# Optimization experiments

Hardware: AMD Instinct MI355X
Metric: run time of the kernel (lower is better)

## Reference

```python
import jax, jax.numpy as jnp
from jax import lax
import numpy as np

H_SIZE = 1024      # max(hidden_size_list)
EXPAND = 2
INTER = EXPAND * H_SIZE            # 2048 intermediate size
NHEADS = 32                        # max(num_heads_list)
HEAD_DIM = INTER // NHEADS         # 64
NSTATE = 128                       # ssm state size
NGROUPS = 1
KCONV = 4                          # conv kernel
CHUNK = 256                        # chunk size for SSD scan
EPS = 1e-5                         # layer_norm_epsilon
CONV_DIM = INTER + 2 * NGROUPS * NSTATE        # 2304
PROJ_DIM = 2 * INTER + 2 * NGROUPS * NSTATE + NHEADS  # 4352


def setup_inputs() -> dict:
    key = jax.random.key(0)
    ks = jax.random.split(key, 9)
    B, S = 2, 4096
    return {
        "hidden_states": jax.random.normal(ks[0], (B, S, H_SIZE), jnp.float32),
        "in_proj_w": jax.random.normal(ks[1], (PROJ_DIM, H_SIZE), jnp.float32) * 0.02,
        "conv_w": jax.random.normal(ks[2], (CONV_DIM, 1, KCONV), jnp.float32) * 0.2,
        "conv_b": jax.random.normal(ks[3], (CONV_DIM,), jnp.float32) * 0.02,
        "dt_bias": jax.random.normal(ks[4], (NHEADS,), jnp.float32) * 0.1,
        "A_log": jax.random.uniform(ks[5], (NHEADS,), jnp.float32, 0.0, 1.0),
        "D": jax.random.normal(ks[6], (NHEADS,), jnp.float32),
        "norm_w": jnp.ones((INTER,), jnp.float32) + 0.01 * jax.random.normal(ks[7], (INTER,), jnp.float32),
        "out_proj_w": jax.random.normal(ks[8], (H_SIZE, INTER), jnp.float32) * 0.02,
    }


def _segsum(a):
    # a: [B,H,C,L] -> lower-triangular segment sums [B,H,C,L,L]
    L = a.shape[-1]
    cs = jnp.cumsum(a, axis=-1)
    ss = cs[..., :, None] - cs[..., None, :]
    mask = jnp.tril(jnp.ones((L, L), dtype=bool))
    return jnp.where(mask, ss, -jnp.inf)


def reference(hidden_states, in_proj_w, conv_w, conv_b, dt_bias, A_log, D, norm_w, out_proj_w):
    B, S, _ = hidden_states.shape
    proj = hidden_states @ in_proj_w.T                       # [B,S,4352]
    gate = proj[..., :INTER]                                 # [B,S,2048]
    hBC = proj[..., INTER:INTER + CONV_DIM]                  # [B,S,2304]
    dt = proj[..., INTER + CONV_DIM:]                        # [B,S,H]

    # causal depthwise conv1d + SiLU
    xc_ = jnp.transpose(hBC, (0, 2, 1))                      # [B,C,S]
    xc_ = lax.conv_general_dilated(xc_, conv_w, (1,), [(KCONV - 1, 0)],
                                   dimension_numbers=('NCH', 'OIH', 'NCH'),
                                   feature_group_count=CONV_DIM)
    xc_ = jax.nn.silu(xc_ + conv_b[None, :, None])
    hBC = jnp.transpose(xc_, (0, 2, 1))                      # [B,S,2304]

    h = hBC[..., :INTER]
    Bm = hBC[..., INTER:INTER + NGROUPS * NSTATE]
    Cm = hBC[..., INTER + NGROUPS * NSTATE:]

    dt = jax.nn.softplus(dt + dt_bias)                       # [B,S,H]
    dt = jnp.clip(dt, 0.0, None)                             # time_step_limit (0, inf)
    A = -jnp.exp(A_log)                                      # [H]

    NC = S // CHUNK
    xh = h.reshape(B, NC, CHUNK, NHEADS, HEAD_DIM)
    Bh = jnp.repeat(Bm.reshape(B, NC, CHUNK, NGROUPS, NSTATE), NHEADS // NGROUPS, axis=3)
    Ch = jnp.repeat(Cm.reshape(B, NC, CHUNK, NGROUPS, NSTATE), NHEADS // NGROUPS, axis=3)
    dtc = dt.reshape(B, NC, CHUNK, NHEADS)

    a = jnp.transpose(dtc * A, (0, 3, 1, 2))                 # [B,H,NC,L]
    A_cum = jnp.cumsum(a, axis=-1)                           # [B,H,NC,L]
    Lmat = jnp.exp(_segsum(a))                               # [B,H,NC,L,L]
    xdt = xh * dtc[..., None]                                # [B,NC,L,H,P]

    # intra-chunk (diagonal block) output
    Yd = jnp.einsum('bclhn,bcshn,bhcls,bcshp->bclhp', Ch, Bh, Lmat, xdt)

    # per-chunk final states
    decay = jnp.exp(A_cum[..., -1:] - A_cum)                 # [B,H,NC,L]
    states = jnp.einsum('bclhn,bhcl,bclhp->bchpn', Bh, decay, xdt)  # [B,NC,H,P,N]

    # inter-chunk recurrence over chunks
    g = jnp.exp(A_cum[..., -1])                              # [B,H,NC]
    def step(carry, inp):
        s_c, g_c = inp
        return carry * g_c[..., None, None] + s_c, carry
    _, prev = lax.scan(step, jnp.zeros((B, NHEADS, HEAD_DIM, NSTATE), states.dtype),
                       (jnp.moveaxis(states, 1, 0), jnp.moveaxis(g, 2, 0)))
    prev = jnp.moveaxis(prev, 0, 1)                          # [B,NC,H,P,N] state entering each chunk

    Yo = jnp.einsum('bclhn,bchpn,bhcl->bclhp', Ch, prev, jnp.exp(A_cum))

    y = (Yd + Yo + D[None, None, None, :, None] * xh).reshape(B, S, INTER)

    # gated RMSNorm (fp32 internally)
    yf = y.astype(jnp.float32) * jax.nn.silu(gate.astype(jnp.float32))
    var = jnp.mean(yf * yf, axis=-1, keepdims=True)
    y = norm_w * (yf * lax.rsqrt(var + EPS))

    return y @ out_proj_w.T
```

## Files before the change

### kernel.cpp

```cpp
#include <hip/hip_runtime.h>
#include <hip/hip_bf16.h>
#include <math.h>

#define H_SIZE   1024
#define INTER    2048
#define NHEADS   32
#define HEAD_DIM 64
#define NSTATE   128
#define KCONV    4
#define CHUNK    256
#define CONV_DIM (INTER + 2*NSTATE)
#define CIN_DIM  (CONV_DIM + NHEADS)
#define PROJ_DIM (2*INTER + 2*NSTATE + NHEADS)
#define BATCH    2
#define SEQ      4096
#define NC       (SEQ/CHUNK)
#define EPS_F    1e-5f

typedef __attribute__((ext_vector_type(8))) short bf16x8;
typedef __attribute__((ext_vector_type(4))) float f32x4;
typedef unsigned short ushort_t;

__device__ __forceinline__ ushort_t f2bf(float x) {
  unsigned u = __float_as_uint(x);
  u += 0x7fffu + ((u >> 16) & 1u);
  return (ushort_t)(u >> 16);
}
__device__ __forceinline__ float bf2f(ushort_t h) {
  return __uint_as_float((unsigned)h << 16);
}

__global__ __launch_bounds__(256) void convert_hl_kernel(
    const float* __restrict__ x, ushort_t* __restrict__ hi,
    ushort_t* __restrict__ lo, int n4) {
  int idx = blockIdx.x * 256 + threadIdx.x;
  int stride = gridDim.x * 256;
  for (int i = idx; i < n4; i += stride) {
    const float* p = x + (size_t)i * 4;
    float v0 = p[0], v1 = p[1], v2 = p[2], v3 = p[3];
    ushort_t h0 = f2bf(v0), h1 = f2bf(v1), h2 = f2bf(v2), h3 = f2bf(v3);
    ushort_t l0 = f2bf(v0 - bf2f(h0));
    ushort_t l1 = f2bf(v1 - bf2f(h1));
    ushort_t l2 = f2bf(v2 - bf2f(h2));
    ushort_t l3 = f2bf(v3 - bf2f(h3));
    *(uint2*)(hi + (size_t)i * 4) =
        make_uint2((unsigned)h0 | ((unsigned)h1 << 16), (unsigned)h2 | ((unsigned)h3 << 16));
    *(uint2*)(lo + (size_t)i * 4) =
        make_uint2((unsigned)l0 | ((unsigned)l1 << 16), (unsigned)l2 | ((unsigned)l3 << 16));
  }
}

__global__ __launch_bounds__(256) void convert_bc_kernel(
    const float* __restrict__ hbc, ushort_t* __restrict__ Bph,
    ushort_t* __restrict__ Bpl, ushort_t* __restrict__ Cph,
    ushort_t* __restrict__ Cpl) {
  const int n4 = (BATCH*SEQ) * 64;
  int idx = blockIdx.x * 256 + threadIdx.x;
  int stride = gridDim.x * 256;
  for (int i = idx; i < n4; i += stride) {
    int row = i >> 6;
    int c4 = (i & 63) * 4;
    float4 v = *(const float4*)(hbc + (size_t)row*CONV_DIM + INTER + c4);
    ushort_t h0 = f2bf(v.x), h1 = f2bf(v.y), h2 = f2bf(v.z), h3 = f2bf(v.w);
    ushort_t l0 = f2bf(v.x - bf2f(h0)), l1 = f2bf(v.y - bf2f(h1));
    ushort_t l2 = f2bf(v.z - bf2f(h2)), l3 = f2bf(v.w - bf2f(h3));
    uint2 hp = make_uint2((unsigned)h0 | ((unsigned)h1 << 16), (unsigned)h2 | ((unsigned)h3 << 16));
    uint2 lp = make_uint2((unsigned)l0 | ((unsigned)l1 << 16), (unsigned)l2 | ((unsigned)l3 << 16));
    if (c4 < 128) {
      *(uint2*)(Bph + (size_t)row*128 + c4) = hp;
      *(uint2*)(Bpl + (size_t)row*128 + c4) = lp;
    } else {
      *(uint2*)(Cph + (size_t)row*128 + (c4 - 128)) = hp;
      *(uint2*)(Cpl + (size_t)row*128 + (c4 - 128)) = lp;
    }
  }
}

#define LROW 40
__global__ __launch_bounds__(256) void gemm_hl_mfma_kernel(
    const ushort_t* __restrict__ Ahi, const ushort_t* __restrict__ Alo,
    const ushort_t* __restrict__ Whi, const ushort_t* __restrict__ Wlo,
    float* __restrict__ C, int M, int N, int K, int nx) {
  __shared__ __align__(16) ushort_t Ah[128*LROW], Al[128*LROW];
  __shared__ __align__(16) ushort_t Wh[128*LROW], Wl[128*LROW];
  const int tid = threadIdx.x;
  const int lane = tid & 63, wid = tid >> 6;
  const int wr = wid >> 1, wc = wid & 1;
  const int fr = lane & 15, fg = lane >> 4;

  const int cpx = gridDim.x >> 3;
  const int logical = (blockIdx.x & 7) * cpx + (blockIdx.x >> 3);
  const int grp = logical / (nx * 4);
  const int rem = logical - grp * (nx * 4);
  const int bx = rem >> 2;
  const int by = grp * 4 + (rem & 3);
  const int m0 = by * 128, n0 = bx * 128;

  const int r0 = tid >> 2;
  const int kseg = (tid & 3) * 8;
  const int r1 = r0 + 64;
  const size_t a0 = (size_t)(m0 + r0) * K + kseg;
  const size_t a1 = (size_t)(m0 + r1) * K + kseg;
  const size_t w0 = (size_t)(n0 + r0) * K + kseg;
  const size_t w1 = (size_t)(n0 + r1) * K + kseg;
  const bool wv0 = (n0 + r0) < N, wv1 = (n0 + r1) < N;

  bf16x8 gA0, gA1, gAl0, gAl1, gW0, gW1, gWl0, gWl1;
  const bf16x8 z8 = {};
  f32x4 acc[4][4] = {};

  auto glod = [&](int k0) {
    gA0  = *(const bf16x8*)(Ahi + a0 + k0);
    gA1  = *(const bf16x8*)(Ahi + a1 + k0);
    gAl0 = *(const bf16x8*)(Alo + a0 + k0);
    gAl1 = *(const bf16x8*)(Alo + a1 + k0);
    gW0  = wv0 ? *(const bf16x8*)(Whi + w0 + k0) : z8;
    gW1  = wv1 ? *(const bf16x8*)(Whi + w1 + k0) : z8;
    gWl0 = wv0 ? *(const bf16x8*)(Wlo + w0 + k0) : z8;
    gWl1 = wv1 ? *(const bf16x8*)(Wlo + w1 + k0) : z8;
  };

  glod(0);
  for (int k0 = 0; k0 < K; k0 += 32) {
    __syncthreads();
    *(bf16x8*)&Ah[r0*LROW + kseg] = gA0;
    *(bf16x8*)&Ah[r1*LROW + kseg] = gA1;
    *(bf16x8*)&Al[r0*LROW + kseg] = gAl0;
    *(bf16x8*)&Al[r1*LROW + kseg] = gAl1;
    *(bf16x8*)&Wh[r0*LROW + kseg] = gW0;
    *(bf16x8*)&Wh[r1*LROW + kseg] = gW1;
    *(bf16x8*)&Wl[r0*LROW + kseg] = gWl0;
    *(bf16x8*)&Wl[r1*LROW + kseg] = gWl1;
    __syncthreads();
    if (k0 + 32 < K) glod(k0 + 32);

    bf16x8 wh[4], wl[4];
#pragma unroll
    for (int nf = 0; nf < 4; ++nf) {
      int off = (wc*64 + nf*16 + fr) * LROW + 8*fg;
      wh[nf] = *(const bf16x8*)&Wh[off];
      wl[nf] = *(const bf16x8*)&Wl[off];
    }
#pragma unroll
    for (int mf = 0; mf < 4; ++mf) {
      int aoff = (wr*64 + mf*16 + fr) * LROW + 8*fg;
      bf16x8 ah = *(const bf16x8*)&Ah[aoff];
      bf16x8 al = *(const bf16x8*)&Al[aoff];
#pragma unroll
      for (int nf = 0; nf < 4; ++nf) {
        acc[mf][nf] = __builtin_amdgcn_mfma_f32_16x16x32_bf16(ah, wh[nf], acc[mf][nf], 0, 0, 0);
        acc[mf][nf] = __builtin_amdgcn_mfma_f32_16x16x32_bf16(ah, wl[nf], acc[mf][nf], 0, 0, 0);
        acc[mf][nf] = __builtin_amdgcn_mfma_f32_16x16x32_bf16(al, wh[nf], acc[mf][nf], 0, 0, 0);
      }
    }
  }

#pragma unroll
  for (int mf = 0; mf < 4; ++mf)
#pragma unroll
    for (int nf = 0; nf < 4; ++nf) {
      int col = n0 + wc*64 + nf*16 + fr;
      if (col < N) {
        size_t base = (size_t)(m0 + wr*64 + mf*16 + fg*4) * N + col;
        f32x4 v = acc[mf][nf];
        C[base]               = v[0];
        C[base + (size_t)N]   = v[1];
        C[base + 2*(size_t)N] = v[2];
        C[base + 3*(size_t)N] = v[3];
      }
    }
}

__global__ __launch_bounds__(256) void conv_kernel(
    const float* __restrict__ cin, const float* __restrict__ cw,
    const float* __restrict__ cb, const float* __restrict__ dtb,
    float* __restrict__ hbc, float* __restrict__ dtp) {
  const int bs = blockIdx.x;
  const int b = bs / SEQ, s = bs % SEQ;
  const int tid = threadIdx.x;
  const float* base = cin + (size_t)b * SEQ * CIN_DIM;
  for (int c = tid; c < CONV_DIM; c += 256) {
    float acc = cb[c];
#pragma unroll
    for (int k = 0; k < KCONV; ++k) {
      int sp = s - (KCONV-1) + k;
      if (sp >= 0) acc = fmaf(cw[c*KCONV + k], base[(size_t)sp * CIN_DIM + c], acc);
    }
    acc = acc / (1.f + expf(-acc));
    hbc[(size_t)bs * CONV_DIM + c] = acc;
  }
  if (tid < NHEADS) {
    float d = cin[(size_t)bs * CIN_DIM + CONV_DIM + tid] + dtb[tid];
    d = (d > 20.f) ? d : log1pf(expf(d));
    dtp[(size_t)bs * NHEADS + tid] = d;
  }
}

__global__ __launch_bounds__(256) void cumsum_kernel(
    const float* __restrict__ dtp, const float* __restrict__ A_log,
    float* __restrict__ acum, float* __restrict__ gch) {
  const int c = blockIdx.x, h = blockIdx.y, b = blockIdx.z;
  const int tid = threadIdx.x;
  __shared__ float sm[CHUNK];
  const float A = -expf(A_log[h]);
  const int s = c * CHUNK + tid;
  float a = dtp[(size_t)(b*SEQ + s)*NHEADS + h] * A;
  sm[tid] = a;
  __syncthreads();
  for (int off = 1; off < CHUNK; off <<= 1) {
    float v = 0.f;
    if (tid >= off) v = sm[tid - off];
    __syncthreads();
    sm[tid] += v;
    __syncthreads();
  }
  float ac = sm[tid];
  acum[((size_t)(b*NHEADS + h)*NC + c)*CHUNK + tid] = ac;
  if (tid == CHUNK-1) gch[(size_t)(b*NHEADS + h)*NC + c] = expf(ac);
}

#define CBROW 136
#define XROW2 72
__global__ __launch_bounds__(256) void yd_mfma_kernel(
    const ushort_t* __restrict__ Bph, const ushort_t* __restrict__ Bpl,
    const ushort_t* __restrict__ Cph, const ushort_t* __restrict__ Cpl,
    const float* __restrict__ hbc, const float* __restrict__ acum,
    const float* __restrict__ dtp, const float* __restrict__ Dv,
    float* __restrict__ y) {
  __shared__ __align__(16) ushort_t BhS[64*CBROW], BlS[64*CBROW];
  __shared__ __align__(16) ushort_t XhS[64*XROW2], XlS[64*XROW2];
  __shared__ __align__(16) ushort_t GhS[4][16*XROW2], GlS[4][16*XROW2];
  __shared__ float acLs[64], acSs[64];

  const int h = blockIdx.x;
  const int c = blockIdx.y >> 2, lt = blockIdx.y & 3;
  const int b = blockIdx.z;
  const int tid = threadIdx.x;
  const int lane = tid & 63, w = tid >> 6;
  const int fr = lane & 15, fg = lane >> 4;

  const size_t seqbase = (size_t)(b*SEQ + c*CHUNK);
  const size_t acbase  = ((size_t)(b*NHEADS + h)*NC + c)*CHUNK;

  bf16x8 cfh[4], cfl[4];
  {
    const size_t cg = (seqbase + lt*64 + w*16 + fr) * 128;
#pragma unroll
    for (int ks = 0; ks < 4; ++ks) {
      int ko = ks*32 + fg*8;
      cfh[ks] = *(const bf16x8*)(Cph + cg + ko);
      cfl[ks] = *(const bf16x8*)(Cpl + cg + ko);
    }
  }
  if (tid < 64) acLs[tid] = acum[acbase + lt*64 + tid];

  f32x4 acc[4] = {};

  for (int st = 0; st <= lt; ++st) {
    __syncthreads();
    {
      const size_t g0 = (seqbase + st*64) * 128;
#pragma unroll
      for (int i = 0; i < 4; ++i) {
        int f = tid + 256*i; int r = f >> 4; int k8 = (f & 15) * 8;
        *(bf16x8*)&BhS[r*CBROW + k8] = *(const bf16x8*)(Bph + g0 + (size_t)r*128 + k8);
        *(bf16x8*)&BlS[r*CBROW + k8] = *(const bf16x8*)(Bpl + g0 + (size_t)r*128 + k8);
      }
    }
#pragma unroll
    for (int i = 0; i < 4; ++i) {
      int f = tid + 256*i; int s = f >> 4; int p0 = (f & 15) * 4;
      size_t row = seqbase + st*64 + s;
      float dtv = dtp[row*NHEADS + h];
      float4 xv = *(const float4*)(hbc + row*CONV_DIM + h*HEAD_DIM + p0);
      float vals[4] = {xv.x*dtv, xv.y*dtv, xv.z*dtv, xv.w*dtv};
#pragma unroll
      for (int j = 0; j < 4; ++j) {
        int p = p0 + j;
        int sw = s ^ (((p >> 2) & 7) << 3);
        ushort_t hh = f2bf(vals[j]);
        ushort_t ll = f2bf(vals[j] - bf2f(hh));
        XhS[p*XROW2 + sw] = hh;
        XlS[p*XROW2 + sw] = ll;
      }
    }
    if (tid < 64) acSs[tid] = acum[acbase + st*64 + tid];
    __syncthreads();

    f32x4 g[4] = {};
#pragma unroll
    for (int ks = 0; ks < 4; ++ks) {
      const int ko = ks*32 + fg*8;
#pragma unroll
      for (int nf = 0; nf < 4; ++nf) {
        const int rb = (nf*16 + fr) * CBROW + ko;
        bf16x8 bh = *(const bf16x8*)&BhS[rb];
        bf16x8 bl = *(const bf16x8*)&BlS[rb];
        g[nf] = __builtin_amdgcn_mfma_f32_16x16x32_bf16(cfh[ks], bh, g[nf], 0, 0, 0);
        g[nf] = __builtin_amdgcn_mfma_f32_16x16x32_bf16(cfh[ks], bl, g[nf], 0, 0, 0);
        g[nf] = __builtin_amdgcn_mfma_f32_16x16x32_bf16(cfl[ks], bh, g[nf], 0, 0, 0);
      }
    }
    {
      const bool full = (st < lt);
#pragma unroll
      for (int nf = 0; nf < 4; ++nf) {
        int sl = nf*16 + fr;
        float aS = acSs[sl];
#pragma unroll
        for (int r = 0; r < 4; ++r) {
          int ll = w*16 + fg*4 + r;
          float v = 0.f;
          if (full || ll >= sl) v = g[nf][r] * __expf(acLs[ll] - aS);
          ushort_t hh = f2bf(v);
          ushort_t lo2 = f2bf(v - bf2f(hh));
          GhS[w][(fg*4 + r)*XROW2 + sl] = hh;
          GlS[w][(fg*4 + r)*XROW2 + sl] = lo2;
        }
      }
    }
    __syncthreads();
#pragma unroll
    for (int ks = 0; ks < 2; ++ks) {
      const int ko = ks*32 + fg*8;
      bf16x8 gh = *(const bf16x8*)&GhS[w][fr*XROW2 + ko];
      bf16x8 gl = *(const bf16x8*)&GlS[w][fr*XROW2 + ko];
#pragma unroll
      for (int nf = 0; nf < 4; ++nf) {
        int p = nf*16 + fr;
        int kb = ko ^ (((p >> 2) & 7) << 3);
        bf16x8 xh = *(const bf16x8*)&XhS[p*XROW2 + kb];
        bf16x8 xl = *(const bf16x8*)&XlS[p*XROW2 + kb];
        acc[nf] = __builtin_amdgcn_mfma_f32_16x16x32_bf16(gh, xh, acc[nf], 0, 0, 0);
        acc[nf] = __builtin_amdgcn_mfma_f32_16x16x32_bf16(gh, xl, acc[nf], 0, 0, 0);
        acc[nf] = __builtin_amdgcn_mfma_f32_16x16x32_bf16(gl, xh, acc[nf], 0, 0, 0);
      }
    }
  }

  const float Dh = Dv[h];
#pragma unroll
  for (int nf = 0; nf < 4; ++nf) {
    int p = nf*16 + fr;
#pragma unroll
    for (int r = 0; r < 4; ++r) {
      size_t row = seqbase + lt*64 + w*16 + fg*4 + r;
      float xval = hbc[row*CONV_DIM + h*HEAD_DIM + p];
      y[row*INTER + h*HEAD_DIM + p] = acc[nf][r] + Dh * xval;
    }
  }
}

#define SXROW 72
__global__ __launch_bounds__(256) void states_mfma_kernel(
    const ushort_t* __restrict__ Bph, const ushort_t* __restrict__ Bpl,
    const float* __restrict__ hbc, const float* __restrict__ acum,
    const float* __restrict__ dtp, float* __restrict__ states) {
  __shared__ __align__(16) ushort_t XhS[64*SXROW], XlS[64*SXROW];
  __shared__ __align__(16) ushort_t BhS[128*SXROW], BlS[128*SXROW];
  const int h = blockIdx.x, c = blockIdx.y, b = blockIdx.z;
  const int tid = threadIdx.x;
  const int lane = tid & 63, w = tid >> 6;
  const int fr = lane & 15, fg = lane >> 4;
  const size_t seqbase = (size_t)(b*SEQ + c*CHUNK);
  const size_t acbase  = ((size_t)(b*NHEADS + h)*NC + c)*CHUNK;
  const float aclast = acum[acbase + CHUNK - 1];
  f32x4 acc[8] = {};

  for (int lt = 0; lt < 4; ++lt) {
    __syncthreads();
#pragma unroll
    for (int i = 0; i < 4; ++i) {
      int f = tid + 256*i; int l = f >> 4; int p0 = (f & 15) * 4;
      size_t row = seqbase + lt*64 + l;
      float mult = dtp[row*NHEADS + h] * __expf(aclast - acum[acbase + lt*64 + l]);
      float4 xv = *(const float4*)(hbc + row*CONV_DIM + h*HEAD_DIM + p0);
      float vals[4] = {xv.x*mult, xv.y*mult, xv.z*mult, xv.w*mult};
#pragma unroll
      for (int j = 0; j < 4; ++j) {
        int p = p0 + j;
        int sw = l ^ (((p >> 2) & 7) << 3);
        ushort_t hh = f2bf(vals[j]);
        XhS[p*SXROW + sw] = hh;
        XlS[p*SXROW + sw] = f2bf(vals[j] - bf2f(hh));
      }
    }
#pragma unroll
    for (int i = 0; i < 4; ++i) {
      int f = tid + 256*i; int l = f >> 4; int n8 = (f & 15) * 8;
      size_t g0 = (seqbase + lt*64 + l) * 128 + n8;
      bf16x8 bh = *(const bf16x8*)(Bph + g0);
      bf16x8 bl = *(const bf16x8*)(Bpl + g0);
#pragma unroll
      for (int j = 0; j < 8; ++j) {
        int n = n8 + j;
        int sw = l ^ (((n >> 2) & 7) << 3);
        BhS[n*SXROW + sw] = (ushort_t)bh[j];
        BlS[n*SXROW + sw] = (ushort_t)bl[j];
      }
    }
    __syncthreads();
#pragma unroll
    for (int ks = 0; ks < 2; ++ks) {
      const int ko = ks*32 + fg*8;
      const int pa = w*16 + fr;
      const int ka = ko ^ (((pa >> 2) & 7) << 3);
      bf16x8 ah = *(const bf16x8*)&XhS[pa*SXROW + ka];
      bf16x8 al = *(const bf16x8*)&XlS[pa*SXROW + ka];
#pragma unroll
      for (int nf = 0; nf < 8; ++nf) {
        const int nb = nf*16 + fr;
        const int kb = ko ^ (((nb >> 2) & 7) << 3);
        bf16x8 bh = *(const bf16x8*)&BhS[nb*SXROW + kb];
        bf16x8 bl = *(const bf16x8*)&BlS[nb*SXROW + kb];
        acc[nf] = __builtin_amdgcn_mfma_f32_16x16x32_bf16(ah, bh, acc[nf], 0, 0, 0);
        acc[nf] = __builtin_amdgcn_mfma_f32_16x16x32_bf16(ah, bl, acc[nf], 0, 0, 0);
        acc[nf] = __builtin_amdgcn_mfma_f32_16x16x32_bf16(al, bh, acc[nf], 0, 0, 0);
      }
    }
  }
  float* sp = states + ((size_t)(b*NC + c)*NHEADS + h)*HEAD_DIM*NSTATE;
#pragma unroll
  for (int nf = 0; nf < 8; ++nf) {
    int n = nf*16 + fr;
#pragma unroll
    for (int r = 0; r < 4; ++r) {
      int p = w*16 + fg*4 + r;
      sp[(size_t)p*NSTATE + n] = acc[nf][r];
    }
  }
}

__global__ __launch_bounds__(256) void scan_kernel(
    float* __restrict__ st, const float* __restrict__ g) {
  const int bh = blockIdx.x;
  const int b = bh >> 5, h = bh & 31;
  const int tid = threadIdx.x;
  float carry[32];
#pragma unroll
  for (int i = 0; i < 32; ++i) carry[i] = 0.f;
  for (int c = 0; c < NC; ++c) {
    const float gc = g[(size_t)(b*NHEADS + h)*NC + c];
    float* base = st + ((size_t)(b*NC + c)*NHEADS + h)*HEAD_DIM*NSTATE;
    ushort_t* ub = (ushort_t*)base;
    float sv[32];
#pragma unroll
    for (int i = 0; i < 32; ++i) sv[i] = base[i*256 + tid];
    __syncthreads();
#pragma unroll
    for (int i = 0; i < 32; ++i) {
      int e = i*256 + tid;
      ushort_t hh = f2bf(carry[i]);
      ub[e]        = hh;
      ub[8192 + e] = f2bf(carry[i] - bf2f(hh));
      carry[i] = fmaf(carry[i], gc, sv[i]);
    }
  }
}

#define PROW 136
__global__ __launch_bounds__(256) void yo_mfma_kernel(
    const ushort_t* __restrict__ Cph, const ushort_t* __restrict__ Cpl,
    const ushort_t* __restrict__ stp, const float* __restrict__ acum,
    float* __restrict__ y) {
  __shared__ __align__(16) ushort_t PhS[64*PROW], PlS[64*PROW];
  const int h = blockIdx.x, c = blockIdx.y, b = blockIdx.z;
  const int tid = threadIdx.x;
  const int lane = tid & 63, w = tid >> 6;
  const int fr = lane & 15, fg = lane >> 4;
  const size_t seqbase = (size_t)(b*SEQ + c*CHUNK);
  const size_t acbase  = ((size_t)(b*NHEADS + h)*NC + c)*CHUNK;

  const ushort_t* pb = stp + ((size_t)(b*NC + c)*NHEADS + h) * (size_t)(2*HEAD_DIM*NSTATE);
#pragma unroll
  for (int i = 0; i < 4; ++i) {
    int f = tid + 256*i; int r = f >> 4; int k8 = (f & 15) * 8;
    *(bf16x8*)&PhS[r*PROW + k8] = *(const bf16x8*)(pb + (size_t)r*128 + k8);
    *(bf16x8*)&PlS[r*PROW + k8] = *(const bf16x8*)(pb + 8192 + (size_t)r*128 + k8);
  }
  __syncthreads();

  for (int lt = 0; lt < 4; ++lt) {
    const size_t cg = (seqbase + lt*64 + w*16 + fr) * 128;
    f32x4 acc[4] = {};
#pragma unroll
    for (int ks = 0; ks < 4; ++ks) {
      int ko = ks*32 + fg*8;
      bf16x8 ah = *(const bf16x8*)(Cph + cg + ko);
      bf16x8 al = *(const bf16x8*)(Cpl + cg + ko);
#pragma unroll
      for (int nf = 0; nf < 4; ++nf) {
        const int rb = (nf*16 + fr) * PROW + ko;
        bf16x8 bh = *(const bf16x8*)&PhS[rb];
        bf16x8 bl = *(const bf16x8*)&PlS[rb];
        acc[nf] = __builtin_amdgcn_mfma_f32_16x16x32_bf16(ah, bh, acc[nf], 0, 0, 0);
        acc[nf] = __builtin_amdgcn_mfma_f32_16x16x32_bf16(ah, bl, acc[nf], 0, 0, 0);
        acc[nf] = __builtin_amdgcn_mfma_f32_16x16x32_bf16(al, bh, acc[nf], 0, 0, 0);
      }
    }
#pragma unroll
    for (int r = 0; r < 4; ++r) {
      int lrow = lt*64 + w*16 + fg*4 + r;
      float e = __expf(acum[acbase + lrow]);
      float* yrow = y + (seqbase + lrow)*INTER + h*HEAD_DIM;
#pragma unroll
      for (int nf = 0; nf < 4; ++nf) {
        int p = nf*16 + fr;
        yrow[p] += e * acc[nf][r];
      }
    }
  }
}

__global__ __launch_bounds__(256) void rms_kernel(
    float* __restrict__ y, const float* __restrict__ gate,
    const float* __restrict__ norm_w) {
  const int bs = blockIdx.x;
  const int tid = threadIdx.x;
  float* yrow = y + (size_t)bs * INTER;
  const float* grow = gate + (size_t)bs * INTER;
  float yf[8];
  float ss = 0.f;
#pragma unroll
  for (int i = 0; i < 8; ++i) {
    int c = tid + i*256;
    float v = yrow[c];
    float gt = grow[c];
    float f = v * (gt / (1.f + expf(-gt)));
    yf[i] = f;
    ss += f*f;
  }
#pragma unroll
  for (int off = 32; off >= 1; off >>= 1) ss += __shfl_xor(ss, off, 64);
  __shared__ float red[4];
  if ((tid & 63) == 0) red[tid >> 6] = ss;
  __syncthreads();
  float total = red[0] + red[1] + red[2] + red[3];
  float sc = rsqrtf(total * (1.f/INTER) + EPS_F);
#pragma unroll
  for (int i = 0; i < 8; ++i) {
    int c = tid + i*256;
    yrow[c] = norm_w[c] * yf[i] * sc;
  }
}

__global__ void zero_kernel(float* p, size_t n) {
  size_t i = (size_t)blockIdx.x * blockDim.x + threadIdx.x;
  if (i < n) p[i] = 0.f;
}

extern "C" void kernel_launch(void* const* d_in, const int* in_sizes, int n_in,
                              void* d_out, int out_size, void* d_ws, size_t ws_size,
                              hipStream_t stream) {
  const float* hidden = (const float*)d_in[0];
  const float* in_w   = (const float*)d_in[1];
  const float* conv_w = (const float*)d_in[2];
  const float* conv_b = (const float*)d_in[3];
  const float* dt_b   = (const float*)d_in[4];
  const float* A_log  = (const float*)d_in[5];
  const float* Dv     = (const float*)d_in[6];
  const float* norm_w = (const float*)d_in[7];
  const float* out_w  = (const float*)d_in[8];
  float* out = (float*)d_out;

  const int M = BATCH*SEQ;

  const size_t sz_cin  = (size_t)M * CIN_DIM;
  const size_t sz_hbc  = (size_t)M * CONV_DIM;
  const size_t sz_dtp  = (size_t)M * NHEADS;
  const size_t sz_acum = (size_t)BATCH*NHEADS*NC*CHUNK;
  const size_t sz_gch  = (size_t)BATCH*NHEADS*NC;
  const size_t sz_R    = (size_t)BATCH*NC*NHEADS*HEAD_DIM*NSTATE;
  const size_t need = (sz_cin + sz_hbc + sz_dtp + sz_acum + sz_gch + sz_R) * sizeof(float);

  if (ws_size < need) {
    size_t n = (size_t)out_size;
    zero_kernel<<<(unsigned)((n + 255) / 256), 256, 0, stream>>>(out, n);
    return;
  }

  float* ws = (float*)d_ws;
  size_t o = 0;
  float* cin  = ws + o; o += sz_cin;
  float* hbc  = ws + o; o += sz_hbc;
  float* dtp  = ws + o; o += sz_dtp;
  float* acum = ws + o; o += sz_acum;
  float* gch  = ws + o; o += sz_gch;
  float* R    = ws + o; o += sz_R;

  float* y    = cin;
  float* gate = hbc;
  float* st   = R;

  ushort_t* hidhi = (ushort_t*)R;
  ushort_t* hidlo = hidhi + (size_t)M * H_SIZE;
  ushort_t* yhi   = (ushort_t*)hbc;
  ushort_t* ylo   = yhi + (size_t)M * INTER;

  ushort_t* wscr = (ushort_t*)out;
  const size_t MP = (size_t)M * 128;
  ushort_t* bcp  = (ushort_t*)((char*)d_out + (size_t)(16u << 20));
  ushort_t* Bph = bcp;
  ushort_t* Bpl = bcp + MP;
  ushort_t* Cph = bcp + 2*MP;
  ushort_t* Cpl = bcp + 3*MP;

  {
    int nA4 = (M * H_SIZE) / 4;
    int nW  = CIN_DIM * H_SIZE;
    int nx = (CIN_DIM + 127) / 128;
    convert_hl_kernel<<<2048, 256, 0, stream>>>(hidden, hidhi, hidlo, nA4);
    convert_hl_kernel<<<2048, 256, 0, stream>>>(in_w + (size_t)INTER*H_SIZE, wscr, wscr + nW, nW/4);
    gemm_hl_mfma_kernel<<<nx * (M/128), 256, 0, stream>>>(
        hidhi, hidlo, wscr, wscr + nW, cin, M, CIN_DIM, H_SIZE, nx);
  }
  conv_kernel<<<dim3(M), 256, 0, stream>>>(cin, conv_w, conv_b, dt_b, hbc, dtp);
  convert_bc_kernel<<<2048, 256, 0, stream>>>(hbc, Bph, Bpl, Cph, Cpl);
  cumsum_kernel<<<dim3(NC, NHEADS, BATCH), 256, 0, stream>>>(dtp, A_log, acum, gch);
  yd_mfma_kernel<<<dim3(NHEADS, NC*4, BATCH), 256, 0, stream>>>(
      Bph, Bpl, Cph, Cpl, hbc, acum, dtp, Dv, y);
  states_mfma_kernel<<<dim3(NHEADS, NC, BATCH), 256, 0, stream>>>(
      Bph, Bpl, hbc, acum, dtp, st);
  scan_kernel<<<dim3(BATCH*NHEADS), 256, 0, stream>>>(st, gch);
  yo_mfma_kernel<<<dim3(NHEADS, NC, BATCH), 256, 0, stream>>>(
      Cph, Cpl, (const ushort_t*)st, acum, y);
  {
    int nA4 = (M * H_SIZE) / 4;
    int nW  = INTER * H_SIZE;
    int nx = INTER / 128;
    convert_hl_kernel<<<2048, 256, 0, stream>>>(hidden, hidhi, hidlo, nA4);
    convert_hl_kernel<<<2048, 256, 0, stream>>>(in_w, wscr, wscr + nW, nW/4);
    gemm_hl_mfma_kernel<<<nx * (M/128), 256, 0, stream>>>(
        hidhi, hidlo, wscr, wscr + nW, gate, M, INTER, H_SIZE, nx);
  }
  rms_kernel<<<dim3(M), 256, 0, stream>>>(y, gate, norm_w);
  {
    int nY4 = (M * INTER) / 4;
    int nW  = H_SIZE * INTER;
    int nx = H_SIZE / 128;
    ushort_t* whi2 = (ushort_t*)R;
    convert_hl_kernel<<<2048, 256, 0, stream>>>(y, yhi, ylo, nY4);
    convert_hl_kernel<<<2048, 256, 0, stream>>>(out_w, whi2, whi2 + nW, nW/4);
    gemm_hl_mfma_kernel<<<nx * (M/128), 256, 0, stream>>>(
        yhi, ylo, whi2, whi2 + nW, out, M, H_SIZE, INTER, nx);
  }
}
```

Measured before the change: 812.1 us.

## Drop activation low-plane in gate and out-proj GEMMs, fuse bf16 cast into RMSNorm

```diff
diff --git a/kernel.cpp b/kernel.cpp
--- a/kernel.cpp
+++ b/kernel.cpp
@@ -77,11 +77,13 @@
 }
 
 #define LROW 40
+template<int PLANES>
 __global__ __launch_bounds__(256) void gemm_hl_mfma_kernel(
     const ushort_t* __restrict__ Ahi, const ushort_t* __restrict__ Alo,
     const ushort_t* __restrict__ Whi, const ushort_t* __restrict__ Wlo,
     float* __restrict__ C, int M, int N, int K, int nx) {
-  __shared__ __align__(16) ushort_t Ah[128*LROW], Al[128*LROW];
+  __shared__ __align__(16) ushort_t Ah[128*LROW];
+  __shared__ __align__(16) ushort_t Al[(PLANES==3) ? 128*LROW : 8];
   __shared__ __align__(16) ushort_t Wh[128*LROW], Wl[128*LROW];
   const int tid = threadIdx.x;
   const int lane = tid & 63, wid = tid >> 6;
@@ -112,8 +114,10 @@
   auto glod = [&](int k0) {
     gA0  = *(const bf16x8*)(Ahi + a0 + k0);
     gA1  = *(const bf16x8*)(Ahi + a1 + k0);
-    gAl0 = *(const bf16x8*)(Alo + a0 + k0);
-    gAl1 = *(const bf16x8*)(Alo + a1 + k0);
+    if constexpr (PLANES == 3) {
+      gAl0 = *(const bf16x8*)(Alo + a0 + k0);
+      gAl1 = *(const bf16x8*)(Alo + a1 + k0);
+    }
     gW0  = wv0 ? *(const bf16x8*)(Whi + w0 + k0) : z8;
     gW1  = wv1 ? *(const bf16x8*)(Whi + w1 + k0) : z8;
     gWl0 = wv0 ? *(const bf16x8*)(Wlo + w0 + k0) : z8;
@@ -125,8 +129,10 @@
     __syncthreads();
     *(bf16x8*)&Ah[r0*LROW + kseg] = gA0;
     *(bf16x8*)&Ah[r1*LROW + kseg] = gA1;
-    *(bf16x8*)&Al[r0*LROW + kseg] = gAl0;
-    *(bf16x8*)&Al[r1*LROW + kseg] = gAl1;
+    if constexpr (PLANES == 3) {
+      *(bf16x8*)&Al[r0*LROW + kseg] = gAl0;
+      *(bf16x8*)&Al[r1*LROW + kseg] = gAl1;
+    }
     *(bf16x8*)&Wh[r0*LROW + kseg] = gW0;
     *(bf16x8*)&Wh[r1*LROW + kseg] = gW1;
     *(bf16x8*)&Wl[r0*LROW + kseg] = gWl0;
@@ -145,12 +151,14 @@
     for (int mf = 0; mf < 4; ++mf) {
       int aoff = (wr*64 + mf*16 + fr) * LROW + 8*fg;
       bf16x8 ah = *(const bf16x8*)&Ah[aoff];
-      bf16x8 al = *(const bf16x8*)&Al[aoff];
+      bf16x8 al;
+      if constexpr (PLANES == 3) al = *(const bf16x8*)&Al[aoff];
 #pragma unroll
       for (int nf = 0; nf < 4; ++nf) {
         acc[mf][nf] = __builtin_amdgcn_mfma_f32_16x16x32_bf16(ah, wh[nf], acc[mf][nf], 0, 0, 0);
         acc[mf][nf] = __builtin_amdgcn_mfma_f32_16x16x32_bf16(ah, wl[nf], acc[mf][nf], 0, 0, 0);
-        acc[mf][nf] = __builtin_amdgcn_mfma_f32_16x16x32_bf16(al, wh[nf], acc[mf][nf], 0, 0, 0);
+        if constexpr (PLANES == 3)
+          acc[mf][nf] = __builtin_amdgcn_mfma_f32_16x16x32_bf16(al, wh[nf], acc[mf][nf], 0, 0, 0);
       }
     }
   }
@@ -431,25 +439,25 @@
   }
 }
 
-__global__ __launch_bounds__(256) void scan_kernel(
+__global__ __launch_bounds__(1024) void scan_kernel(
     float* __restrict__ st, const float* __restrict__ g) {
   const int bh = blockIdx.x;
   const int b = bh >> 5, h = bh & 31;
   const int tid = threadIdx.x;
-  float carry[32];
-#pragma unroll
-  for (int i = 0; i < 32; ++i) carry[i] = 0.f;
+  float carry[8];
+#pragma unroll
+  for (int i = 0; i < 8; ++i) carry[i] = 0.f;
   for (int c = 0; c < NC; ++c) {
     const float gc = g[(size_t)(b*NHEADS + h)*NC + c];
     float* base = st + ((size_t)(b*NC + c)*NHEADS + h)*HEAD_DIM*NSTATE;
     ushort_t* ub = (ushort_t*)base;
-    float sv[32];
-#pragma unroll
-    for (int i = 0; i < 32; ++i) sv[i] = base[i*256 + tid];
-    __syncthreads();
-#pragma unroll
-    for (int i = 0; i < 32; ++i) {
-      int e = i*256 + tid;
+    float sv[8];
+#pragma unroll
+    for (int i = 0; i < 8; ++i) sv[i] = base[i*1024 + tid];
+    __syncthreads();
+#pragma unroll
+    for (int i = 0; i < 8; ++i) {
+      int e = i*1024 + tid;
       ushort_t hh = f2bf(carry[i]);
       ub[e]        = hh;
       ub[8192 + e] = f2bf(carry[i] - bf2f(hh));
@@ -513,11 +521,11 @@
 }
 
 __global__ __launch_bounds__(256) void rms_kernel(
-    float* __restrict__ y, const float* __restrict__ gate,
-    const float* __restrict__ norm_w) {
+    const float* __restrict__ y, const float* __restrict__ gate,
+    const float* __restrict__ norm_w, ushort_t* __restrict__ yh) {
   const int bs = blockIdx.x;
   const int tid = threadIdx.x;
-  float* yrow = y + (size_t)bs * INTER;
+  const float* yrow = y + (size_t)bs * INTER;
   const float* grow = gate + (size_t)bs * INTER;
   float yf[8];
   float ss = 0.f;
@@ -540,7 +548,7 @@
 #pragma unroll
   for (int i = 0; i < 8; ++i) {
     int c = tid + i*256;
-    yrow[c] = norm_w[c] * yf[i] * sc;
+    yh[(size_t)bs*INTER + c] = f2bf(norm_w[c] * yf[i] * sc);
   }
 }
 
@@ -594,8 +602,8 @@
 
   ushort_t* hidhi = (ushort_t*)R;
   ushort_t* hidlo = hidhi + (size_t)M * H_SIZE;
-  ushort_t* yhi   = (ushort_t*)hbc;
-  ushort_t* ylo   = yhi + (size_t)M * INTER;
+  ushort_t* yhR   = (ushort_t*)R;
+  ushort_t* wplh  = (ushort_t*)hbc;
 
   ushort_t* wscr = (ushort_t*)out;
   const size_t MP = (size_t)M * 128;
@@ -611,7 +619,7 @@
     int nx = (CIN_DIM + 127) / 128;
     convert_hl_kernel<<<2048, 256, 0, stream>>>(hidden, hidhi, hidlo, nA4);
     convert_hl_kernel<<<2048, 256, 0, stream>>>(in_w + (size_t)INTER*H_SIZE, wscr, wscr + nW, nW/4);
-    gemm_hl_mfma_kernel<<<nx * (M/128), 256, 0, stream>>>(
+    gemm_hl_mfma_kernel<3><<<nx * (M/128), 256, 0, stream>>>(
         hidhi, hidlo, wscr, wscr + nW, cin, M, CIN_DIM, H_SIZE, nx);
   }
   conv_kernel<<<dim3(M), 256, 0, stream>>>(cin, conv_w, conv_b, dt_b, hbc, dtp);
@@ -621,7 +629,7 @@
       Bph, Bpl, Cph, Cpl, hbc, acum, dtp, Dv, y);
   states_mfma_kernel<<<dim3(NHEADS, NC, BATCH), 256, 0, stream>>>(
       Bph, Bpl, hbc, acum, dtp, st);
-  scan_kernel<<<dim3(BATCH*NHEADS), 256, 0, stream>>>(st, gch);
+  scan_kernel<<<dim3(BATCH*NHEADS), 1024, 0, stream>>>(st, gch);
   yo_mfma_kernel<<<dim3(NHEADS, NC, BATCH), 256, 0, stream>>>(
       Cph, Cpl, (const ushort_t*)st, acum, y);
   {
@@ -630,18 +638,15 @@
     int nx = INTER / 128;
     convert_hl_kernel<<<2048, 256, 0, stream>>>(hidden, hidhi, hidlo, nA4);
     convert_hl_kernel<<<2048, 256, 0, stream>>>(in_w, wscr, wscr + nW, nW/4);
-    gemm_hl_mfma_kernel<<<nx * (M/128), 256, 0, stream>>>(
+    gemm_hl_mfma_kernel<2><<<nx * (M/128), 256, 0, stream>>>(
         hidhi, hidlo, wscr, wscr + nW, gate, M, INTER, H_SIZE, nx);
   }
-  rms_kernel<<<dim3(M), 256, 0, stream>>>(y, gate, norm_w);
+  rms_kernel<<<dim3(M), 256, 0, stream>>>(y, gate, norm_w, yhR);
   {
-    int nY4 = (M * INTER) / 4;
     int nW  = H_SIZE * INTER;
+    convert_hl_kernel<<<2048, 256, 0, stream>>>(out_w, wplh, wplh + nW, nW/4);
     int nx = H_SIZE / 128;
-    ushort_t* whi2 = (ushort_t*)R;
-    convert_hl_kernel<<<2048, 256, 0, stream>>>(y, yhi, ylo, nY4);
-    convert_hl_kernel<<<2048, 256, 0, stream>>>(out_w, whi2, whi2 + nW, nW/4);
-    gemm_hl_mfma_kernel<<<nx * (M/128), 256, 0, stream>>>(
-        yhi, ylo, whi2, whi2 + nW, out, M, H_SIZE, INTER, nx);
-  }
-}
+    gemm_hl_mfma_kernel<2><<<nx * (M/128), 256, 0, stream>>>(
+        yhR, yhR, wplh, wplh + nW, out, M, H_SIZE, INTER, nx);
+  }
+}
```

Measured after the change: 735.0 us. -9.5%, faster.
